# Performance work log

Measured on AMD Instinct MI355X. Metric: run time of the kernel, lower is better.

Reference implementation:

```python
import jax, jax.numpy as jnp
import numpy as np

DICT_LEN = 9
NUM_LS = 8
DIM = 1024
SEQ = 2048
BZ = 32


def setup_inputs() -> dict:
    key = jax.random.key(0)
    k_x, k_ids, k_w, k_b = jax.random.split(key, 4)
    x = jax.random.normal(k_x, (SEQ, BZ, DIM), dtype=jnp.float32)
    lang_ids = jax.random.randint(k_ids, (BZ,), 0, DICT_LEN)
    # torch nn.Linear init: U(-1/sqrt(in), 1/sqrt(in)), weight shape [out, in]
    bound = 1.0 / np.sqrt(DIM)
    W = jax.random.uniform(k_w, (NUM_LS, DIM, DIM), dtype=jnp.float32, minval=-bound, maxval=bound)
    b = jax.random.uniform(k_b, (NUM_LS, DIM), dtype=jnp.float32, minval=-bound, maxval=bound)
    return {"x": x, "lang_ids": lang_ids, "W": W, "b": b}


def reference(x, lang_ids, W, b):
    # Mapper.forward: gid = dict_len - 1 - lang_ids; tokens with gid in [1, num_ls]
    # are transformed by Linear #(gid-1); all other batch columns pass through.
    gid = DICT_LEN - 1 - lang_ids                      # [bz]
    active = (gid >= 1) & (gid <= NUM_LS)              # [bz]
    eidx = jnp.clip(gid - 1, 0, NUM_LS - 1)            # [bz] expert index (dummy 0 where inactive)
    We = W[eidx]                                       # [bz, dim, dim] (torch Linear weight layout [out, in])
    be = b[eidx]                                       # [bz, dim]
    y = jnp.einsum("sbd,bed->sbe", x, We) + be[None, :, :]
    return jnp.where(active[None, :, None], y, x)
```

## Files before the change

### kernel.cpp

```cpp
#include <hip/hip_runtime.h>
#include <hip/hip_bf16.h>

#define TSEQ 2048
#define TBZ  32
#define TDIM 1024
#define NLS  8

typedef __attribute__((ext_vector_type(8))) short bf16x8;
typedef __attribute__((ext_vector_type(4))) float f32x4;

__device__ inline unsigned int pk2(float lo, float hi) {
    __hip_bfloat162 h = __float22bfloat162_rn(make_float2(lo, hi));
    return *reinterpret_cast<const unsigned int*>(&h);
}

__device__ inline void gload_lds16(const void* g, void* l) {
    __builtin_amdgcn_global_load_lds(
        (const __attribute__((address_space(1))) unsigned int*)g,
        (__attribute__((address_space(3))) unsigned int*)l,
        16, 0, 0);
}

__global__ __launch_bounds__(256) void conv_all(
    const float* __restrict__ x, const int* __restrict__ lang_ids,
    const float* __restrict__ W,
    unsigned short* __restrict__ xb, unsigned short* __restrict__ wb,
    float* __restrict__ out)
{
    const int bid = blockIdx.x;
    if (bid < 256) {
        const int total = NLS * TDIM * TDIM / 8;
        for (int i = bid * 256 + threadIdx.x; i < total; i += 256 * 256) {
            const float* src = W + (long)i * 8;
            f32x4 v0 = *(const f32x4*)(src);
            f32x4 v1 = *(const f32x4*)(src + 4);
            uint4 o;
            o.x = pk2(v0.x, v0.y); o.y = pk2(v0.z, v0.w);
            o.z = pk2(v1.x, v1.y); o.w = pk2(v1.z, v1.w);
            *(uint4*)(wb + (long)i * 8) = o;
        }
        return;
    }
    const int xb_id = bid - 256;
    const int b     = xb_id >> 6;
    const int s0c   = (xb_id & 63) * 32;
    const int gid   = 8 - lang_ids[b];
    const bool active = (gid >= 1) && (gid <= 8);

    for (int i = threadIdx.x; i < 32 * 128; i += 256) {
        const int ls = i >> 7;
        const int d8 = i & 127;
        const int s  = s0c + ls;
        const float* src = x + ((long)s * TBZ + b) * TDIM + d8 * 8;
        f32x4 v0 = *(const f32x4*)(src);
        f32x4 v1 = *(const f32x4*)(src + 4);
        if (active) {
            uint4 o;
            o.x = pk2(v0.x, v0.y); o.y = pk2(v0.z, v0.w);
            o.z = pk2(v1.x, v1.y); o.w = pk2(v1.z, v1.w);
            *(uint4*)(xb + ((long)b * TSEQ + s) * TDIM + d8 * 8) = o;
        } else {
            float* dst = out + ((long)s * TBZ + b) * TDIM + d8 * 8;
            *(f32x4*)(dst)     = v0;
            *(f32x4*)(dst + 4) = v1;
        }
    }
}


#define BAR __builtin_amdgcn_s_barrier()
#define SB0 __builtin_amdgcn_sched_barrier(0)
#define VMC(n) asm volatile("s_waitcnt vmcnt(" #n ")" ::: "memory")
#define KAo(kv) (((kv) & 1023) + (((kv) >> 10) << 18))
#define KBo(kv) ((kv) & 1023)

__global__ __launch_bounds__(512, 2) void mapper_gemm8p(
    const unsigned short* __restrict__ xb,
    const int* __restrict__ lang_ids,
    const unsigned short* __restrict__ wb,
    const float* __restrict__ bias,
    float* __restrict__ out)
{
    const int p  = blockIdx.x;
    const int l  = (p & 7) * 32 + (p >> 3);
    const int b  = l >> 3;
    const int strip = (l >> 2) & 1;
    const int nt = l & 3;
    const int s0 = strip * 1024;
    const int e0 = nt * 256;
    const int tid = threadIdx.x;

    const int gid = 8 - lang_ids[b];
    if (!(gid >= 1 && gid <= 8)) return;
    const int eb = gid - 1;

    __shared__ uint4 ldsbuf[131072 / 16];
    char* ldsc = (char*)ldsbuf;

    const int lane = tid & 63;
    const int wave = tid >> 6;
    const int wr   = wave >> 2;
    const int wc   = wave & 3;
    const int fr   = lane & 15;
    const int fq   = lane >> 4;
    const int fr7  = fr & 7;

    const unsigned short* __restrict__ Aab = xb + (long)b  * TSEQ * TDIM + (long)s0 * TDIM;
    const unsigned short* __restrict__ Bbb = wb + (long)eb * TDIM * TDIM + (long)e0 * TDIM;

    const int L    = lane;
    const int lch8 = ((L & 7) ^ (L >> 3)) * 8;
    const int ldA0 = wave * 2048 + L * 16;
    const unsigned short* aG[2][2];
    const unsigned short* bG[2][2];
    #pragma unroll
    for (int j = 0; j < 2; ++j) {
        const int rr = wave * 16 + j * 8 + (L >> 3);
        #pragma unroll
        for (int mh = 0; mh < 2; ++mh)
            aG[j][mh] = Aab + ((rr >> 6) * 128 + mh * 64 + (rr & 63)) * TDIM + lch8;
        #pragma unroll
        for (int nh = 0; nh < 2; ++nh)
            bG[j][nh] = Bbb + ((rr >> 5) * 64 + nh * 32 + (rr & 31)) * TDIM + lch8;
    }

#define STAGE_A(slot, mh, kofs) do { \
    gload_lds16(aG[0][mh] + (kofs), ldsc + (slot)*32768 + (mh)*16384 + ldA0); \
    gload_lds16(aG[1][mh] + (kofs), ldsc + (slot)*32768 + (mh)*16384 + ldA0 + 1024); \
} while (0)
#define STAGE_B(slot, nh, kofs) do { \
    gload_lds16(bG[0][nh] + (kofs), ldsc + 65536 + (slot)*32768 + (nh)*16384 + ldA0); \
    gload_lds16(bG[1][nh] + (kofs), ldsc + 65536 + (slot)*32768 + (nh)*16384 + ldA0 + 1024); \
} while (0)
#define RD_A(slot, mh) do { \
    _Pragma("unroll") for (int ml = 0; ml < 4; ++ml) { \
        const int rr = wr * 64 + ml * 16 + fr; \
        _Pragma("unroll") for (int kk = 0; kk < 2; ++kk) \
            af[ml][kk] = *(const bf16x8*)(ldsc + (slot)*32768 + (mh)*16384 + rr*128 + (((kk*4+fq) ^ fr7) << 4)); \
    } } while (0)
#define RD_B(slot, nh, br) do { \
    _Pragma("unroll") for (int nl = 0; nl < 2; ++nl) { \
        const int rr = wc * 32 + nl * 16 + fr; \
        _Pragma("unroll") for (int kk = 0; kk < 2; ++kk) \
            br[nl][kk] = *(const bf16x8*)(ldsc + 65536 + (slot)*32768 + (nh)*16384 + rr*128 + (((kk*4+fq) ^ fr7) << 4)); \
    } } while (0)
#define MM(mh, nh, br) do { \
    __builtin_amdgcn_s_setprio(1); \
    _Pragma("unroll") for (int ml = 0; ml < 4; ++ml) \
    _Pragma("unroll") for (int nl = 0; nl < 2; ++nl) \
    _Pragma("unroll") for (int kk = 0; kk < 2; ++kk) \
        acc[(mh)*4+ml][(nh)*2+nl] = __builtin_amdgcn_mfma_f32_16x16x32_bf16( \
            br[nl][kk], af[ml][kk], acc[(mh)*4+ml][(nh)*2+nl], 0, 0, 0); \
    __builtin_amdgcn_s_setprio(0); \
} while (0)

    f32x4 acc[8][4];
    #pragma unroll
    for (int m = 0; m < 8; ++m)
        #pragma unroll
        for (int n = 0; n < 4; ++n)
            acc[m][n] = (f32x4){0.f, 0.f, 0.f, 0.f};

    bf16x8 af[4][2], bf0[2][2], bf1[2][2];

    STAGE_A(0, 0, 0);  STAGE_B(0, 0, 0);  STAGE_B(0, 1, 0);  STAGE_A(0, 1, 0);
    STAGE_A(1, 0, 64); STAGE_B(1, 0, 64); STAGE_B(1, 1, 64);
    VMC(6); BAR; SB0;

    const int cs  = lane & 15;
    const int eqb = (lane >> 4) << 2;

    #pragma unroll 1
    for (int mtl = 0; mtl < 4; ++mtl) {
        #pragma unroll 1
        for (int it = 0; it < 8; ++it) {
            const int kva = mtl * 1024 + it * 128;
            const int kb = kva + 64;
            const int kn = kva + 128;
            const int km = kva + 192;
            RD_A(0, 0); RD_B(0, 0, bf0); STAGE_A(1, 1, KAo(kb));
            BAR; SB0; MM(0, 0, bf0); BAR; SB0;
            RD_B(0, 1, bf1); STAGE_A(0, 0, KAo(kn));
            BAR; SB0; MM(0, 1, bf1); BAR; SB0;
            RD_A(0, 1); STAGE_B(0, 0, KBo(kn));
            BAR; SB0; MM(1, 0, bf0); BAR; SB0;
            STAGE_B(0, 1, KBo(kn));
            BAR; SB0; MM(1, 1, bf1); VMC(6); BAR; SB0;
            RD_A(1, 0); RD_B(1, 0, bf0); STAGE_A(0, 1, KAo(kn));
            BAR; SB0; MM(0, 0, bf0); BAR; SB0;
            RD_B(1, 1, bf1); STAGE_A(1, 0, KAo(km));
            BAR; SB0; MM(0, 1, bf1); BAR; SB0;
            RD_A(1, 1); STAGE_B(1, 0, KBo(km));
            BAR; SB0; MM(1, 0, bf0); BAR; SB0;
            STAGE_B(1, 1, KBo(km));
            BAR; SB0; MM(1, 1, bf1); VMC(6); BAR; SB0;
        }

        const int sb = s0 + mtl * 256 + wr * 128;
        #pragma unroll
        for (int n = 0; n < 4; ++n) {
            const int e = e0 + wc * 64 + n * 16 + eqb;
            const f32x4 bv4 = *(const f32x4*)&bias[eb * TDIM + e];
            #pragma unroll
            for (int m = 0; m < 8; ++m) {
                const int s = sb + m * 16 + cs;
                *(f32x4*)&out[(long)s * (TBZ * TDIM) + b * TDIM + e] = acc[m][n] + bv4;
            }
        }
        #pragma unroll
        for (int m = 0; m < 8; ++m)
            #pragma unroll
            for (int n = 0; n < 4; ++n)
                acc[m][n] = (f32x4){0.f, 0.f, 0.f, 0.f};
    }
#undef STAGE_A
#undef STAGE_B
#undef RD_A
#undef RD_B
#undef MM
}

__device__ inline unsigned short f2bf(float f) {
    union { float f; unsigned int u; } v; v.f = f;
    unsigned int r = v.u + 0x7fffu + ((v.u >> 16) & 1u);
    return (unsigned short)(r >> 16);
}
constexpr int FLDS = 40;

__global__ __launch_bounds__(256) void mapper_fused(
    const float* __restrict__ x, const int* __restrict__ lang_ids,
    const float* __restrict__ W, const float* __restrict__ bias,
    float* __restrict__ out)
{
    const int bid = blockIdx.x;
    const int b   = bid >> 7;
    const int t   = bid & 127;
    const int mt  = t >> 3;
    const int nt  = t & 7;
    const int s0  = mt * 128;
    const int e0  = nt * 128;
    const int tid = threadIdx.x;

    const int gid = 8 - lang_ids[b];
    const bool active = (gid >= 1) && (gid <= 8);
    int eb = gid - 1; eb = eb < 0 ? 0 : (eb > 7 ? 7 : eb);

    if (!active) {
        const f32x4* xs = (const f32x4*)x;
        f32x4*       os = (f32x4*)out;
        const int rs4 = TBZ * TDIM / 4;
        for (int i = tid; i < 128 * 128 / 4; i += 256) {
            int r = i >> 5, c = i & 31;
            long idx = (long)(s0 + r) * rs4 + b * (TDIM / 4) + (e0 >> 2) + c;
            os[idx] = xs[idx];
        }
        return;
    }

    __shared__ unsigned short As[128 * FLDS];
    __shared__ unsigned short Bs[128 * FLDS];
    const float* __restrict__ Wb = W + (long)eb * TDIM * TDIM;

    const int lane = tid & 63;
    const int wave = tid >> 6;
    const int wrr  = wave >> 1;
    const int wcc  = wave & 1;

    f32x4 acc[4][4];
    #pragma unroll
    for (int m = 0; m < 4; ++m)
        #pragma unroll
        for (int n = 0; n < 4; ++n)
            acc[m][n] = (f32x4){0.f, 0.f, 0.f, 0.f};

    const int rg = tid >> 3;
    const int cg = tid & 7;
    const int fr = lane & 15;
    const int fo = (lane >> 4) * 8;

    for (int k0 = 0; k0 < TDIM; k0 += 32) {
        __syncthreads();
        #pragma unroll
        for (int pp = 0; pp < 4; ++pp) {
            const int r = rg + pp * 32;
            f32x4 av = *(const f32x4*)(x  + (long)(s0 + r) * (TBZ * TDIM) + b * TDIM + k0 + cg * 4);
            f32x4 bv = *(const f32x4*)(Wb + (long)(e0 + r) * TDIM + k0 + cg * 4);
            unsigned int alo = (unsigned)f2bf(av.x) | ((unsigned)f2bf(av.y) << 16);
            unsigned int ahi = (unsigned)f2bf(av.z) | ((unsigned)f2bf(av.w) << 16);
            unsigned int blo = (unsigned)f2bf(bv.x) | ((unsigned)f2bf(bv.y) << 16);
            unsigned int bhi = (unsigned)f2bf(bv.z) | ((unsigned)f2bf(bv.w) << 16);
            *(uint2*)&As[r * FLDS + cg * 4] = make_uint2(alo, ahi);
            *(uint2*)&Bs[r * FLDS + cg * 4] = make_uint2(blo, bhi);
        }
        __syncthreads();

        bf16x8 af2[4], bfm[4];
        #pragma unroll
        for (int m = 0; m < 4; ++m)
            af2[m] = *(const bf16x8*)&As[(wrr * 64 + m * 16 + fr) * FLDS + fo];
        #pragma unroll
        for (int n = 0; n < 4; ++n)
            bfm[n] = *(const bf16x8*)&Bs[(wcc * 64 + n * 16 + fr) * FLDS + fo];
        #pragma unroll
        for (int m = 0; m < 4; ++m)
            #pragma unroll
            for (int n = 0; n < 4; ++n)
                acc[m][n] = __builtin_amdgcn_mfma_f32_16x16x32_bf16(af2[m], bfm[n], acc[m][n], 0, 0, 0);
    }

    const int cr = lane >> 4;
    const int cc2 = lane & 15;
    #pragma unroll
    for (int n = 0; n < 4; ++n) {
        const int e  = e0 + wcc * 64 + n * 16 + cc2;
        const float bv = bias[eb * TDIM + e];
        #pragma unroll
        for (int m = 0; m < 4; ++m) {
            #pragma unroll
            for (int j = 0; j < 4; ++j) {
                const int s = s0 + wrr * 64 + m * 16 + cr * 4 + j;
                out[(long)s * (TBZ * TDIM) + b * TDIM + e] = acc[m][n][j] + bv;
            }
        }
    }
}

extern "C" void kernel_launch(void* const* d_in, const int* in_sizes, int n_in,
                              void* d_out, int out_size, void* d_ws, size_t ws_size,
                              hipStream_t stream) {
    const float* x        = (const float*)d_in[0];
    const int*   lang_ids = (const int*)d_in[1];
    const float* W        = (const float*)d_in[2];
    const float* bias     = (const float*)d_in[3];
    float*       out      = (float*)d_out;

    const size_t xbytes = (size_t)TSEQ * TBZ * TDIM * 2;
    const size_t wbytes = (size_t)NLS * TDIM * TDIM * 2;

    if (ws_size >= xbytes + wbytes) {
        unsigned short* xbp = (unsigned short*)d_ws;
        unsigned short* wbp = (unsigned short*)((char*)d_ws + xbytes);
        conv_all<<<2304, 256, 0, stream>>>(x, lang_ids, W, xbp, wbp, out);
        mapper_gemm8p<<<256, 512, 0, stream>>>(xbp, lang_ids, wbp, bias, out);
    } else {
        mapper_fused<<<TBZ * 16 * 8, 256, 0, stream>>>(x, lang_ids, W, bias, out);
    }
}
```

Measured before the change: 259.6 us.

## Overlap x bf16 conversion with GEMM via per-strip flags; passthrough in GEMM

The pre-pass now converts only the first 256-row chunk of each active batch strip, plus W, and zeroes a small flag array. The GEMM kernel's blocks convert later x chunks themselves during the K loop. They signal completion with release atomics, and other blocks spin on an acquire load before staging those rows. Inactive batch columns are copied to the output by the GEMM blocks instead of the pre-pass. This moves most x conversion off the critical path, at the cost of inter-block spin-waits that depend on co-residency and of added work inside the main loop.

```diff
diff --git a/kernel.cpp b/kernel.cpp
--- a/kernel.cpp
+++ b/kernel.cpp
@@ -21,13 +21,17 @@
         16, 0, 0);
 }
 
-__global__ __launch_bounds__(256) void conv_all(
+__global__ __launch_bounds__(256) void conv_pre(
     const float* __restrict__ x, const int* __restrict__ lang_ids,
     const float* __restrict__ W,
     unsigned short* __restrict__ xb, unsigned short* __restrict__ wb,
-    float* __restrict__ out)
+    int* __restrict__ flags)
 {
     const int bid = blockIdx.x;
+    if (bid == 512) {
+        if (threadIdx.x < 256) flags[threadIdx.x] = 0;
+        return;
+    }
     if (bid < 256) {
         const int total = NLS * TDIM * TDIM / 8;
         for (int i = bid * 256 + threadIdx.x; i < total; i += 256 * 256) {
@@ -41,29 +45,19 @@
         }
         return;
     }
-    const int xb_id = bid - 256;
-    const int b     = xb_id >> 6;
-    const int s0c   = (xb_id & 63) * 32;
-    const int gid   = 8 - lang_ids[b];
-    const bool active = (gid >= 1) && (gid <= 8);
-
-    for (int i = threadIdx.x; i < 32 * 128; i += 256) {
-        const int ls = i >> 7;
-        const int d8 = i & 127;
-        const int s  = s0c + ls;
-        const float* src = x + ((long)s * TBZ + b) * TDIM + d8 * 8;
-        f32x4 v0 = *(const f32x4*)(src);
-        f32x4 v1 = *(const f32x4*)(src + 4);
-        if (active) {
-            uint4 o;
-            o.x = pk2(v0.x, v0.y); o.y = pk2(v0.z, v0.w);
-            o.z = pk2(v1.x, v1.y); o.w = pk2(v1.z, v1.w);
-            *(uint4*)(xb + ((long)b * TSEQ + s) * TDIM + d8 * 8) = o;
-        } else {
-            float* dst = out + ((long)s * TBZ + b) * TDIM + d8 * 8;
-            *(f32x4*)(dst)     = v0;
-            *(f32x4*)(dst + 4) = v1;
-        }
+    const int i  = bid - 256;
+    const int c  = i >> 2;
+    const int q  = i & 3;
+    const int b  = c >> 1;
+    const int gid = 8 - lang_ids[b];
+    if (!(gid >= 1 && gid <= 8)) return;
+    const int srow0 = (c & 1) * 4 * 256 + q * 64;
+    for (int r = 0; r < 64; ++r) {
+        const int s = srow0 + r;
+        const float* sp = x + ((long)s * TBZ + b) * TDIM + threadIdx.x * 4;
+        f32x4 v = *(const f32x4*)sp;
+        uint2 o; o.x = pk2(v.x, v.y); o.y = pk2(v.z, v.w);
+        *(uint2*)(xb + ((long)b * TSEQ + s) * TDIM + threadIdx.x * 4) = o;
     }
 }
 
@@ -75,10 +69,12 @@
 #define KBo(kv) ((kv) & 1023)
 
 __global__ __launch_bounds__(512, 2) void mapper_gemm8p(
-    const unsigned short* __restrict__ xb,
+    const float* __restrict__ x,
+    unsigned short* xb,
     const int* __restrict__ lang_ids,
     const unsigned short* __restrict__ wb,
     const float* __restrict__ bias,
+    int* flags,
     float* __restrict__ out)
 {
     const int p  = blockIdx.x;
@@ -91,7 +87,18 @@
     const int tid = threadIdx.x;
 
     const int gid = 8 - lang_ids[b];
-    if (!(gid >= 1 && gid <= 8)) return;
+    if (!(gid >= 1 && gid <= 8)) {
+        const f32x4* xs = (const f32x4*)x;
+        f32x4*       os = (f32x4*)out;
+        const int rs4 = TBZ * TDIM / 4;
+        for (int i = tid; i < 1024 * 256 / 4; i += 512) {
+            int r = i >> 6;
+            int c = i & 63;
+            long idx = (long)(s0 + r) * rs4 + b * (TDIM / 4) + (e0 >> 2) + c;
+            os[idx] = xs[idx];
+        }
+        return;
+    }
     const int eb = gid - 1;
 
     __shared__ uint4 ldsbuf[131072 / 16];
@@ -105,7 +112,7 @@
     const int fq   = lane >> 4;
     const int fr7  = fr & 7;
 
-    const unsigned short* __restrict__ Aab = xb + (long)b  * TSEQ * TDIM + (long)s0 * TDIM;
+    const unsigned short* Aab = xb + (long)b  * TSEQ * TDIM + (long)s0 * TDIM;
     const unsigned short* __restrict__ Bbb = wb + (long)eb * TDIM * TDIM + (long)e0 * TDIM;
 
     const int L    = lane;
@@ -154,6 +161,24 @@
     __builtin_amdgcn_s_setprio(0); \
 } while (0)
 
+#define CONVQ(mt) do { \
+    const int sbase_ = (mt) * 256 + nt * 64 + wave * 8; \
+    _Pragma("unroll 1") for (int r_ = 0; r_ < 8; ++r_) { \
+        const int s_ = sbase_ + r_; \
+        const float* sp_ = x + ((long)s_ * TBZ + b) * TDIM + lane * 16; \
+        f32x4 a0_ = *(const f32x4*)(sp_);      f32x4 a1_ = *(const f32x4*)(sp_ + 4); \
+        f32x4 a2_ = *(const f32x4*)(sp_ + 8);  f32x4 a3_ = *(const f32x4*)(sp_ + 12); \
+        uint4 o0_, o1_; \
+        o0_.x = pk2(a0_.x, a0_.y); o0_.y = pk2(a0_.z, a0_.w); \
+        o0_.z = pk2(a1_.x, a1_.y); o0_.w = pk2(a1_.z, a1_.w); \
+        o1_.x = pk2(a2_.x, a2_.y); o1_.y = pk2(a2_.z, a2_.w); \
+        o1_.z = pk2(a3_.x, a3_.y); o1_.w = pk2(a3_.z, a3_.w); \
+        unsigned short* dp_ = xb + ((long)b * TSEQ + s_) * TDIM + lane * 16; \
+        *(uint4*)(dp_)     = o0_; \
+        *(uint4*)(dp_ + 8) = o1_; \
+    } \
+} while (0)
+
     f32x4 acc[8][4];
     #pragma unroll
     for (int m = 0; m < 8; ++m)
@@ -162,6 +187,8 @@
             acc[m][n] = (f32x4){0.f, 0.f, 0.f, 0.f};
 
     bf16x8 af[4][2], bf0[2][2], bf1[2][2];
+
+    const int flbase = (b * 2 + strip) * 4;
 
     STAGE_A(0, 0, 0);  STAGE_B(0, 0, 0);  STAGE_B(0, 1, 0);  STAGE_A(0, 1, 0);
     STAGE_A(1, 0, 64); STAGE_B(1, 0, 64); STAGE_B(1, 1, 64);
@@ -174,6 +201,17 @@
     for (int mtl = 0; mtl < 4; ++mtl) {
         #pragma unroll 1
         for (int it = 0; it < 8; ++it) {
+            if (it == 7 && mtl < 3) {
+                if (lane == 0) {
+                    while (__hip_atomic_load(&flags[flbase + mtl + 1],
+                                             __ATOMIC_RELAXED,
+                                             __HIP_MEMORY_SCOPE_AGENT) < 4)
+                        __builtin_amdgcn_s_sleep(2);
+                }
+                __hip_atomic_load(&flags[flbase + mtl + 1],
+                                  __ATOMIC_ACQUIRE, __HIP_MEMORY_SCOPE_AGENT);
+                SB0;
+            }
             const int kva = mtl * 1024 + it * 128;
             const int kb = kva + 64;
             const int kn = kva + 128;
@@ -185,7 +223,11 @@
             RD_A(0, 1); STAGE_B(0, 0, KBo(kn));
             BAR; SB0; MM(1, 0, bf0); BAR; SB0;
             STAGE_B(0, 1, KBo(kn));
-            BAR; SB0; MM(1, 1, bf1); VMC(6); BAR; SB0;
+            BAR; SB0; MM(1, 1, bf1); VMC(6);
+            if (it == 1 && mtl < 3 && tid == 0)
+                __hip_atomic_fetch_add(&flags[flbase + mtl + 1], 1,
+                                       __ATOMIC_RELEASE, __HIP_MEMORY_SCOPE_AGENT);
+            BAR; SB0;
             RD_A(1, 0); RD_B(1, 0, bf0); STAGE_A(0, 1, KAo(kn));
             BAR; SB0; MM(0, 0, bf0); BAR; SB0;
             RD_B(1, 1, bf1); STAGE_A(1, 0, KAo(km));
@@ -193,7 +235,9 @@
             RD_A(1, 1); STAGE_B(1, 0, KBo(km));
             BAR; SB0; MM(1, 0, bf0); BAR; SB0;
             STAGE_B(1, 1, KBo(km));
-            BAR; SB0; MM(1, 1, bf1); VMC(6); BAR; SB0;
+            BAR; SB0; MM(1, 1, bf1); VMC(6); SB0;
+            if (it == 0 && mtl < 3) { CONVQ(strip * 4 + mtl + 1); }
+            BAR; SB0;
         }
 
         const int sb = s0 + mtl * 256 + wr * 128;
@@ -218,6 +262,7 @@
 #undef RD_A
 #undef RD_B
 #undef MM
+#undef CONVQ
 }
 
 __device__ inline unsigned short f2bf(float f) {
@@ -336,12 +381,14 @@
 
     const size_t xbytes = (size_t)TSEQ * TBZ * TDIM * 2;
     const size_t wbytes = (size_t)NLS * TDIM * TDIM * 2;
-
-    if (ws_size >= xbytes + wbytes) {
+    const size_t fbytes = 1024;
+
+    if (ws_size >= xbytes + wbytes + fbytes) {
         unsigned short* xbp = (unsigned short*)d_ws;
         unsigned short* wbp = (unsigned short*)((char*)d_ws + xbytes);
-        conv_all<<<2304, 256, 0, stream>>>(x, lang_ids, W, xbp, wbp, out);
-        mapper_gemm8p<<<256, 512, 0, stream>>>(xbp, lang_ids, wbp, bias, out);
+        int*            flg = (int*)((char*)d_ws + xbytes + wbytes);
+        conv_pre<<<513, 256, 0, stream>>>(x, lang_ids, W, xbp, wbp, flg);
+        mapper_gemm8p<<<256, 512, 0, stream>>>(x, xbp, lang_ids, wbp, bias, flg, out);
     } else {
         mapper_fused<<<TBZ * 16 * 8, 256, 0, stream>>>(x, lang_ids, W, bias, out);
     }
```

Measured after the change: 302.6 us. 16.6% more time.
